# Performance work log

Hardware: AMD Instinct MI355X
Metric: run time of the kernel (lower is better)

The kernel has to match this reference:

```python
import jax, jax.numpy as jnp
import numpy as np

N = 50000      # nodes
E = 600000     # edges
G = 8          # graphs in the batch (for mean_nodes)
D = 128        # input_dim == hidden_dim
OUT = 10       # out_dim
NEG_SLOPE = 0.01  # nn.LeakyReLU default


def _lin(k, fi, fo):
    return jax.random.normal(k, (fi, fo), jnp.float32) / np.sqrt(fi).astype(np.float32)


def setup_inputs() -> dict:
    key = jax.random.key(0)
    ks = jax.random.split(key, 12)
    inputs = jax.random.normal(ks[0], (N, D), jnp.float32)
    src = jax.random.randint(ks[1], (E,), 0, N)
    dst = jax.random.randint(ks[2], (E,), 0, N)
    graph_id = jnp.sort(jax.random.randint(ks[3], (N,), 0, G))
    return {
        "inputs": inputs,
        "src": src,
        "dst": dst,
        "graph_id": graph_id,
        # GraphConv weights (DGL GraphConv: y = norm * A_norm x W + b)
        "W1": _lin(ks[4], D, D), "b1": jnp.zeros((D,), jnp.float32),
        "W2": _lin(ks[5], D, D), "b2": jnp.zeros((D,), jnp.float32),
        "W3": _lin(ks[6], D, D), "b3": jnp.zeros((D,), jnp.float32),
        # classifier head
        "Wc1": _lin(ks[7], D, 512),  "bc1": jnp.zeros((512,), jnp.float32),
        "Wc2": _lin(ks[8], 512, 256), "bc2": jnp.zeros((256,), jnp.float32),
        "Wc3": _lin(ks[9], 256, OUT), "bc3": jnp.zeros((OUT,), jnp.float32),
    }


def reference(inputs, src, dst, graph_id, W1, b1, W2, b2, W3, b3,
              Wc1, bc1, Wc2, bc2, Wc3, bc3):
    # DGL GraphConv with norm='both': h = D_in^{-1/2} A D_out^{-1/2} x W + b
    ones_e = jnp.ones((E,), jnp.float32)
    out_deg = jax.ops.segment_sum(ones_e, src, num_segments=N)
    in_deg = jax.ops.segment_sum(ones_e, dst, num_segments=N)
    src_norm = jnp.clip(out_deg, 1.0, None) ** -0.5   # [N]
    dst_norm = jnp.clip(in_deg, 1.0, None) ** -0.5    # [N]

    def gconv(x, W, b):
        x = x * src_norm[:, None]
        x = x @ W                                      # project first (in>=out)
        agg = jax.ops.segment_sum(x[src], dst, num_segments=N)  # SpMM
        return agg * dst_norm[:, None] + b

    h = gconv(inputs, W1, b1)
    h = gconv(h, W2, b2)
    h = gconv(h, W3, b3)

    # dgl.mean_nodes: per-graph mean over nodes
    sums = jax.ops.segment_sum(h, graph_id, num_segments=G)         # [G, D]
    cnts = jax.ops.segment_sum(jnp.ones((N,), jnp.float32), graph_id, num_segments=G)
    pooled = sums / jnp.clip(cnts, 1.0, None)[:, None]

    lrelu = lambda v: jax.nn.leaky_relu(v, NEG_SLOPE)
    x = lrelu(pooled @ Wc1 + bc1)
    x = lrelu(x @ Wc2 + bc2)
    x = lrelu(x @ Wc3 + bc3)
    return x
```

## Files before the change

kernel.cpp:

```cpp
#include <hip/hip_runtime.h>

#define Nn 50000
#define Ee 600000
#define Gg 8
#define Dd 128
#define NP 50048
#define SCHUNK 1024
#define NCHUNK ((Nn + SCHUNK - 1) / SCHUNK)

#define HWORDS 25024
#define HB 16
#define HIST_BLOCKS (2 * HB)
#define W12_BLOCKS 16
#define RN_BLOCKS ((HWORDS + 255) / 256)
#define W123_BLOCKS 64
#define PBLK ((Nn + 127) / 128)

__global__ __launch_bounds__(1024) void hist_kernel(
    const int* __restrict__ src, const int* __restrict__ dst,
    unsigned int* __restrict__ phist,
    const float* __restrict__ W1, const float* __restrict__ W2,
    const float* __restrict__ W3, const float* __restrict__ b1,
    const float* __restrict__ b2,
    float* __restrict__ W12, float* __restrict__ e1, float* __restrict__ e2,
    float* __restrict__ accz)
{
    __shared__ unsigned int h[HWORDS];
    int t = threadIdx.x;
    int b = blockIdx.x;

    if (b < HIST_BLOCKS) {
        for (int i = t; i < HWORDS; i += 1024) h[i] = 0u;
        __syncthreads();
        int part = b >> 1;
        const int* arr = (b & 1) ? dst : src;
        int e0 = part * (Ee / HB);
        int eN = e0 + (Ee / HB);
        for (int e = e0 + t; e < eN; e += 1024) {
            int n = arr[e];
            atomicAdd(&h[n >> 1], 1u << ((n & 1) << 4));
        }
        __syncthreads();
        unsigned int* out = phist + (size_t)b * HWORDS;
        for (int i = t; i < HWORDS; i += 1024) out[i] = h[i];
    } else if (b < HIST_BLOCKS + W12_BLOCKS) {
        int j = (b - HIST_BLOCKS) * 8 + (t & 7);
        int k = t >> 3;
        float a = 0.f;
#pragma unroll 8
        for (int m = 0; m < 128; ++m) a += W1[k * 128 + m] * W2[m * 128 + j];
        W12[k * 128 + j] = a;
    } else {
        if (t < 128) {
            float a = 0.f;
#pragma unroll 8
            for (int k = 0; k < 128; ++k) a += b1[k] * W2[k * 128 + t];
            e1[t] = a;
        } else if (t < 256) {
            int c = t - 128;
            float a = 0.f;
#pragma unroll 8
            for (int k = 0; k < 128; ++k) a += b2[k] * W3[k * 128 + c];
            e2[c] = a;
        } else if (t < 256 + 24) {
            accz[t - 256] = 0.f;
        }
    }
}

__global__ __launch_bounds__(256) void reduce_norm_kernel(
    const unsigned int* __restrict__ phist, const int* __restrict__ gid,
    int* __restrict__ odeg, float* __restrict__ srcn, float* __restrict__ pq,
    float* __restrict__ z, int* __restrict__ cnt,
    const float* __restrict__ W12, const float* __restrict__ W3,
    const float* __restrict__ e1,
    float* __restrict__ W123, float* __restrict__ e1b)
{
    int b = blockIdx.x, t = threadIdx.x;
    if (b < RN_BLOCKS) {
        __shared__ int lc[Gg];
        if (t < Gg) lc[t] = 0;
        __syncthreads();
        int i = b * 256 + t;
        if (i < HWORDS) {
            unsigned int so0 = 0, so1 = 0, si0 = 0, si1 = 0;
#pragma unroll
            for (int p = 0; p < HB; ++p) {
                unsigned int a = phist[(size_t)(2 * p) * HWORDS + i];
                unsigned int bb = phist[(size_t)(2 * p + 1) * HWORDS + i];
                so0 += a & 0xffffu; so1 += a >> 16;
                si0 += bb & 0xffffu; si1 += bb >> 16;
            }
#pragma unroll
            for (int hh = 0; hh < 2; ++hh) {
                int n = 2 * i + hh;
                unsigned int so = hh ? so1 : so0, si = hh ? si1 : si0;
                if (n < Nn) {
                    odeg[n] = (int)so;
                    float sn = 1.f / sqrtf(fmaxf((float)so, 1.f));
                    float dn = 1.f / sqrtf(fmaxf((float)si, 1.f));
                    srcn[n] = sn; pq[n] = sn * dn;
                    int g = gid[n];
                    atomicAdd(&lc[g], 1);
                    float zr[8];
#pragma unroll
                    for (int gg = 0; gg < 8; ++gg) zr[gg] = (gg == g) ? dn : 0.f;
                    *(float4*)(z + (size_t)n * 8)     = *(float4*)zr;
                    *(float4*)(z + (size_t)n * 8 + 4) = *(float4*)(zr + 4);
                }
            }
        }
        __syncthreads();
        if (t < Gg && lc[t] > 0) atomicAdd(&cnt[t], lc[t]);
    } else if (b < RN_BLOCKS + W123_BLOCKS) {
        int j = (b - RN_BLOCKS) * 2 + (t & 1);
        int k = t >> 1;
        float a = 0.f;
#pragma unroll 8
        for (int m = 0; m < 128; ++m) a += W12[k * 128 + m] * W3[m * 128 + j];
        W123[k * 128 + j] = a;
    } else {
        if (t < 128) {
            float a = 0.f;
#pragma unroll 8
            for (int k = 0; k < 128; ++k) a += e1[k] * W3[k * 128 + t];
            e1b[t] = a;
        }
    }
}

__global__ __launch_bounds__(256) void scanA(
    const int* __restrict__ deg, int* __restrict__ row_ptr, int* __restrict__ bsum)
{
    __shared__ int tsum[256];
    int b = blockIdx.x, t = threadIdx.x;
    int base = b * SCHUNK + t * 4;
    int v[4]; int s = 0;
#pragma unroll
    for (int i = 0; i < 4; ++i) {
        int idx = base + i;
        v[i] = (idx < Nn) ? deg[idx] : 0;
        s += v[i];
    }
    tsum[t] = s;
    __syncthreads();
    for (int off = 1; off < 256; off <<= 1) {
        int x = (t >= off) ? tsum[t - off] : 0;
        __syncthreads();
        tsum[t] += x;
        __syncthreads();
    }
    int run = tsum[t] - s;
#pragma unroll
    for (int i = 0; i < 4; ++i) {
        int idx = base + i;
        if (idx < Nn) row_ptr[idx] = run;
        run += v[i];
    }
    if (t == 255) bsum[b] = tsum[255];
}

__global__ void scanB(int* __restrict__ bsum)
{
    int t = threadIdx.x;
    int v = (t < NCHUNK) ? bsum[t] : 0;
    int orig = v;
    for (int off = 1; off < 64; off <<= 1) {
        int x = __shfl_up(v, off, 64);
        if (t >= off) v += x;
    }
    if (t < NCHUNK) bsum[t] = v - orig;
}

__global__ __launch_bounds__(256) void scanC(
    int* __restrict__ row_ptr, const int* __restrict__ bsum, int* __restrict__ cursor)
{
    int n = blockIdx.x * 256 + threadIdx.x;
    if (n >= Nn) return;
    int v = row_ptr[n] + bsum[n / SCHUNK];
    row_ptr[n] = v;
    cursor[n] = v;
    if (n == 0) row_ptr[Nn] = Ee;
}

__global__ __launch_bounds__(256) void fill_kernel(
    const int* __restrict__ src, const int* __restrict__ dst,
    int* __restrict__ cursor, int* __restrict__ csr_dst)
{
    int e = blockIdx.x * 256 + threadIdx.x;
    if (e >= Ee) return;
    int pos = atomicAdd(&cursor[src[e]], 1);
    csr_dst[pos] = dst[e];
}

__global__ __launch_bounds__(256) void bspmm_kernel(
    const float* __restrict__ uin, const int* __restrict__ row_ptr,
    const int* __restrict__ csr, const float* __restrict__ scal,
    float* __restrict__ uout, const float* __restrict__ sn,
    float* __restrict__ pwout)
{
    int t = threadIdx.x;
    int m = blockIdx.x * 32 + (t >> 3);
    int g = t & 7;
    float acc = 0.f, snm = 0.f;
    if (m < Nn) {
        int beg = row_ptr[m], end = row_ptr[m + 1];
        float a0 = 0.f, a1 = 0.f;
        int j = beg;
        if (scal) {
            for (; j + 1 < end; j += 2) {
                int i0 = csr[j], i1 = csr[j + 1];
                a0 += scal[i0] * uin[(size_t)i0 * 8 + g];
                a1 += scal[i1] * uin[(size_t)i1 * 8 + g];
            }
            if (j < end) { int i0 = csr[j]; a0 += scal[i0] * uin[(size_t)i0 * 8 + g]; }
        } else {
            for (; j + 1 < end; j += 2) {
                int i0 = csr[j], i1 = csr[j + 1];
                a0 += uin[(size_t)i0 * 8 + g];
                a1 += uin[(size_t)i1 * 8 + g];
            }
            if (j < end) a0 += uin[(size_t)csr[j] * 8 + g];
        }
        acc = a0 + a1;
        uout[(size_t)m * 8 + g] = acc;
        if (pwout) snm = sn[m];
    }
    if (pwout) {
        __shared__ float red[Gg];
        if (t < Gg) red[t] = 0.f;
        __syncthreads();
        atomicAdd(&red[g], snm * acc);
        __syncthreads();
        if (t < Gg) atomicAdd(&pwout[t], red[t]);
    }
}

__global__ __launch_bounds__(256) void dotpool_kernel(
    const float* __restrict__ x, const float* __restrict__ u3,
    const float* __restrict__ sn, float* __restrict__ partial)
{
    __shared__ float f[128][Gg];
    __shared__ float sp[Gg][Dd];
    int t = threadIdx.x;
    int n0 = blockIdx.x * 128;
    if (t < 128) {
        int n = n0 + t;
        float s = 0.f;
        float4 a = {0.f, 0.f, 0.f, 0.f}, b = {0.f, 0.f, 0.f, 0.f};
        if (n < Nn) {
            s = sn[n];
            a = *(const float4*)(u3 + (size_t)n * 8);
            b = *(const float4*)(u3 + (size_t)n * 8 + 4);
        }
        f[t][0] = s * a.x; f[t][1] = s * a.y; f[t][2] = s * a.z; f[t][3] = s * a.w;
        f[t][4] = s * b.x; f[t][5] = s * b.y; f[t][6] = s * b.z; f[t][7] = s * b.w;
    }
    for (int i = t; i < Gg * Dd; i += 256) ((float*)sp)[i] = 0.f;
    __syncthreads();

    int r0 = t >> 5, c = t & 31;
    float4 acc[Gg];
#pragma unroll
    for (int g = 0; g < Gg; ++g) acc[g] = make_float4(0.f, 0.f, 0.f, 0.f);
    for (int i = r0; i < 128; i += 8) {
        int n = n0 + i;
        if (n >= Nn) break;
        float4 xv = ((const float4*)x)[(size_t)n * 32 + c];
#pragma unroll
        for (int g = 0; g < Gg; ++g) {
            float fv = f[i][g];
            acc[g].x += fv * xv.x; acc[g].y += fv * xv.y;
            acc[g].z += fv * xv.z; acc[g].w += fv * xv.w;
        }
    }
#pragma unroll
    for (int g = 0; g < Gg; ++g) {
        atomicAdd(&sp[g][c * 4 + 0], acc[g].x);
        atomicAdd(&sp[g][c * 4 + 1], acc[g].y);
        atomicAdd(&sp[g][c * 4 + 2], acc[g].z);
        atomicAdd(&sp[g][c * 4 + 3], acc[g].w);
    }
    __syncthreads();
    float* out = partial + (size_t)blockIdx.x * Gg * Dd;
    for (int i = t; i < Gg * Dd; i += 256) out[i] = ((float*)sp)[i];
}

__global__ __launch_bounds__(256) void dotreduce_kernel(
    const float* __restrict__ partial, float* __restrict__ pooled)
{
    int i = blockIdx.x * 256 + threadIdx.x;
    float a0 = 0.f, a1 = 0.f, a2 = 0.f, a3 = 0.f;
    int b = 0;
    for (; b + 3 < PBLK; b += 4) {
        a0 += partial[(size_t)(b + 0) * Gg * Dd + i];
        a1 += partial[(size_t)(b + 1) * Gg * Dd + i];
        a2 += partial[(size_t)(b + 2) * Gg * Dd + i];
        a3 += partial[(size_t)(b + 3) * Gg * Dd + i];
    }
    for (; b < PBLK; ++b) a0 += partial[(size_t)b * Gg * Dd + i];
    pooled[i] = (a0 + a1) + (a2 + a3);
}

__global__ __launch_bounds__(1024) void x0_kernel(
    const float* __restrict__ pooled, const float* __restrict__ pw1r,
    const float* __restrict__ pw2r, const int* __restrict__ cnt,
    const float* __restrict__ W123, const float* __restrict__ e1b,
    const float* __restrict__ e2, const float* __restrict__ b3,
    float* __restrict__ x0g)
{
    int t = threadIdx.x;
    int g = t >> 7, c = t & 127;
    float a = 0.f;
#pragma unroll 8
    for (int k = 0; k < 128; ++k) a += pooled[g * 128 + k] * W123[k * 128 + c];
    float inv = 1.f / fmaxf((float)cnt[g], 1.f);
    x0g[t] = a * inv + (pw2r[g] * inv) * e1b[c] + (pw1r[g] * inv) * e2[c] + b3[c];
}

__global__ __launch_bounds__(256) void fc1_kernel(
    const float* __restrict__ x0g, const float* __restrict__ Wc1,
    const float* __restrict__ bc1, float* __restrict__ x1g)
{
    __shared__ float xs[Gg * 128];
    __shared__ float par[256];
    int t = threadIdx.x;
    for (int i = t; i < Gg * 128; i += 256) xs[i] = x0g[i];
    __syncthreads();
    int h = t >> 7, rem = t & 127;
    int g = rem >> 4, m = blockIdx.x * 16 + (rem & 15);
    int k0 = h * 64;
    float a = 0.f;
#pragma unroll 16
    for (int k = 0; k < 64; ++k) a += xs[g * 128 + k0 + k] * Wc1[(size_t)(k0 + k) * 512 + m];
    par[t] = a;
    __syncthreads();
    if (t < 128) {
        float v = par[t] + par[t + 128] + bc1[m];
        x1g[g * 512 + m] = v > 0.f ? v : 0.01f * v;
    }
}

__global__ __launch_bounds__(256) void fc2_kernel(
    const float* __restrict__ x1g, const float* __restrict__ Wc2,
    const float* __restrict__ bc2, float* __restrict__ x2g)
{
    __shared__ float xs[Gg * 512];
    __shared__ float par[256];
    int t = threadIdx.x;
    for (int i = t; i < Gg * 512; i += 256) xs[i] = x1g[i];
    __syncthreads();
    int q = t >> 6, rem = t & 63;
    int g = rem >> 3, m = blockIdx.x * 8 + (rem & 7);
    int k0 = q * 128;
    float a = 0.f;
#pragma unroll 16
    for (int k = 0; k < 128; ++k) a += xs[g * 512 + k0 + k] * Wc2[(size_t)(k0 + k) * 256 + m];
    par[t] = a;
    __syncthreads();
    if (t < 64) {
        float v = par[t] + par[t + 64] + par[t + 128] + par[t + 192] + bc2[m];
        x2g[g * 256 + m] = v > 0.f ? v : 0.01f * v;
    }
}

__global__ __launch_bounds__(640) void fc3_kernel(
    const float* __restrict__ x2g, const float* __restrict__ Wc3,
    const float* __restrict__ bc3, float* __restrict__ out)
{
    __shared__ float xs[Gg * 256];
    int t = threadIdx.x;
    for (int i = t; i < Gg * 256; i += 640) xs[i] = x2g[i];
    __syncthreads();
    int w = t >> 6, lane = t & 63;
    if (w < 10) {
        float acc[Gg];
#pragma unroll
        for (int g = 0; g < Gg; ++g) acc[g] = 0.f;
#pragma unroll
        for (int kk = 0; kk < 4; ++kk) {
            int k = lane + kk * 64;
            float wv = Wc3[(size_t)k * 10 + w];
#pragma unroll
            for (int g = 0; g < Gg; ++g) acc[g] += xs[g * 256 + k] * wv;
        }
#pragma unroll
        for (int g = 0; g < Gg; ++g) {
            float v = acc[g];
            for (int off = 32; off; off >>= 1) v += __shfl_down(v, off, 64);
            if (lane == 0) {
                v += bc3[w];
                out[g * 10 + w] = v > 0.f ? v : 0.01f * v;
            }
        }
    }
}

extern "C" void kernel_launch(void* const* d_in, const int* in_sizes, int n_in,
                              void* d_out, int out_size, void* d_ws, size_t ws_size,
                              hipStream_t stream)
{
    const float* inputs = (const float*)d_in[0];
    const int*   src    = (const int*)d_in[1];
    const int*   dst    = (const int*)d_in[2];
    const int*   gid    = (const int*)d_in[3];
    const float* W1  = (const float*)d_in[4];
    const float* b1  = (const float*)d_in[5];
    const float* W2  = (const float*)d_in[6];
    const float* b2  = (const float*)d_in[7];
    const float* W3  = (const float*)d_in[8];
    const float* b3  = (const float*)d_in[9];
    const float* Wc1 = (const float*)d_in[10];
    const float* bc1 = (const float*)d_in[11];
    const float* Wc2 = (const float*)d_in[12];
    const float* bc2 = (const float*)d_in[13];
    const float* Wc3 = (const float*)d_in[14];
    const float* bc3 = (const float*)d_in[15];

    int*   wi      = (int*)d_ws;
    int*   odeg    = wi;
    int*   row_ptr = odeg + NP;
    int*   cursor  = row_ptr + NP;
    int*   bsum    = cursor + NP;
    int*   csr_dst = bsum + 64;
    float* wf      = (float*)(csr_dst + Ee);
    float* srcn    = wf;
    float* pq      = srcn + NP;
    float* z       = pq + NP;
    float* u1      = z + (size_t)NP * 8;
    float* u2      = u1 + (size_t)NP * 8;
    float* u3      = u2 + (size_t)NP * 8;
    float* partial = u3 + (size_t)NP * 8;
    float* pooled  = partial + (size_t)PBLK * Gg * Dd;
    float* pw1     = pooled + Gg * Dd;
    float* pw2     = pw1 + Gg;
    int*   cnt     = (int*)(pw2 + Gg);
    float* W12v    = (float*)(cnt + Gg);
    float* W123v   = W12v + 128 * 128;
    float* e1v     = W123v + 128 * 128;
    float* e1bv    = e1v + 128;
    float* e2v     = e1bv + 128;
    float* x0g     = e2v + 128;
    float* x1g     = x0g + Gg * 128;
    float* x2g     = x1g + Gg * 512;
    unsigned int* phist = (unsigned int*)(x2g + Gg * 256);

    hist_kernel<<<HIST_BLOCKS + W12_BLOCKS + 1, 1024, 0, stream>>>(
        src, dst, phist, W1, W2, W3, b1, b2, W12v, e1v, e2v, pw1);
    reduce_norm_kernel<<<RN_BLOCKS + W123_BLOCKS + 1, 256, 0, stream>>>(
        phist, gid, odeg, srcn, pq, z, cnt, W12v, W3, e1v, W123v, e1bv);
    scanA<<<NCHUNK, 256, 0, stream>>>(odeg, row_ptr, bsum);
    scanB<<<1, 64, 0, stream>>>(bsum);
    scanC<<<(Nn + 255) / 256, 256, 0, stream>>>(row_ptr, bsum, cursor);
    fill_kernel<<<(Ee + 255) / 256, 256, 0, stream>>>(src, dst, cursor, csr_dst);

    int bblocks = (Nn + 31) / 32;
    bspmm_kernel<<<bblocks, 256, 0, stream>>>(z, row_ptr, csr_dst, nullptr,
                                              u1, srcn, pw1);
    bspmm_kernel<<<bblocks, 256, 0, stream>>>(u1, row_ptr, csr_dst, pq,
                                              u2, srcn, pw2);
    bspmm_kernel<<<bblocks, 256, 0, stream>>>(u2, row_ptr, csr_dst, pq,
                                              u3, nullptr, nullptr);

    dotpool_kernel<<<PBLK, 256, 0, stream>>>(inputs, u3, srcn, partial);
    dotreduce_kernel<<<4, 256, 0, stream>>>(partial, pooled);

    x0_kernel<<<1, 1024, 0, stream>>>(pooled, pw1, pw2, cnt, W123v, e1bv, e2v,
                                      b3, x0g);
    fc1_kernel<<<32, 256, 0, stream>>>(x0g, Wc1, bc1, x1g);
    fc2_kernel<<<32, 256, 0, stream>>>(x1g, Wc2, bc2, x2g);
    fc3_kernel<<<1, 640, 0, stream>>>(x2g, Wc3, bc3, (float*)d_out);
}
```

Baseline: 198.3 us.

## Fuse degree reduce with decoupled-lookback scan and fold third SpMM into pooling

Merges the degree-reduction/normalisation kernel with a single-pass scan that uses per-block flags and serial lookback, replacing three separate scan kernels. The third sparse aggregation is computed inside the pooling kernel, so u3 is never materialised, and the partial reduction is merged into the x0 projection kernel. This cuts several launches and global round trips. In exchange, correctness relies on earlier blocks running forward (spin-wait on flags), and the flags are zeroed in the hist kernel.

```diff
diff --git a/kernel.cpp b/kernel.cpp
--- a/kernel.cpp
+++ b/kernel.cpp
@@ -5,14 +5,12 @@
 #define Gg 8
 #define Dd 128
 #define NP 50048
-#define SCHUNK 1024
-#define NCHUNK ((Nn + SCHUNK - 1) / SCHUNK)
+#define NCHUNK 49
 
 #define HWORDS 25024
 #define HB 16
 #define HIST_BLOCKS (2 * HB)
 #define W12_BLOCKS 16
-#define RN_BLOCKS ((HWORDS + 255) / 256)
 #define W123_BLOCKS 64
 #define PBLK ((Nn + 127) / 128)
 
@@ -23,7 +21,7 @@
     const float* __restrict__ W3, const float* __restrict__ b1,
     const float* __restrict__ b2,
     float* __restrict__ W12, float* __restrict__ e1, float* __restrict__ e2,
-    float* __restrict__ accz)
+    int* __restrict__ accz)
 {
     __shared__ unsigned int h[HWORDS];
     int t = threadIdx.x;
@@ -62,41 +60,51 @@
 #pragma unroll 8
             for (int k = 0; k < 128; ++k) a += b2[k] * W3[k * 128 + c];
             e2[c] = a;
-        } else if (t < 256 + 24) {
-            accz[t - 256] = 0.f;
-        }
-    }
-}
-
-__global__ __launch_bounds__(256) void reduce_norm_kernel(
+        } else if (t < 256 + 88) {
+            accz[t - 256] = 0;
+        }
+    }
+}
+
+__global__ __launch_bounds__(256) void scan_fused(
     const unsigned int* __restrict__ phist, const int* __restrict__ gid,
-    int* __restrict__ odeg, float* __restrict__ srcn, float* __restrict__ pq,
-    float* __restrict__ z, int* __restrict__ cnt,
+    float* __restrict__ srcn, float* __restrict__ pq, float* __restrict__ z,
+    int* __restrict__ cnt, int* __restrict__ row_ptr, int* __restrict__ cursor,
+    int* __restrict__ fs,
     const float* __restrict__ W12, const float* __restrict__ W3,
     const float* __restrict__ e1,
     float* __restrict__ W123, float* __restrict__ e1b)
 {
     int b = blockIdx.x, t = threadIdx.x;
-    if (b < RN_BLOCKS) {
+    if (b < NCHUNK) {
+        __shared__ int tsum[256];
         __shared__ int lc[Gg];
+        __shared__ int sbase;
         if (t < Gg) lc[t] = 0;
         __syncthreads();
-        int i = b * 256 + t;
-        if (i < HWORDS) {
-            unsigned int so0 = 0, so1 = 0, si0 = 0, si1 = 0;
-#pragma unroll
-            for (int p = 0; p < HB; ++p) {
-                unsigned int a = phist[(size_t)(2 * p) * HWORDS + i];
-                unsigned int bb = phist[(size_t)(2 * p + 1) * HWORDS + i];
-                so0 += a & 0xffffu; so1 += a >> 16;
-                si0 += bb & 0xffffu; si1 += bb >> 16;
+
+        int d4[4];
+        int wbase = b * 512 + t * 2;
+#pragma unroll
+        for (int wi = 0; wi < 2; ++wi) {
+            int w = wbase + wi;
+            unsigned so0 = 0, so1 = 0, si0 = 0, si1 = 0;
+            if (w < HWORDS) {
+#pragma unroll
+                for (int p = 0; p < HB; ++p) {
+                    unsigned a  = phist[(size_t)(2 * p) * HWORDS + w];
+                    unsigned bb = phist[(size_t)(2 * p + 1) * HWORDS + w];
+                    so0 += a & 0xffffu; so1 += a >> 16;
+                    si0 += bb & 0xffffu; si1 += bb >> 16;
+                }
             }
 #pragma unroll
             for (int hh = 0; hh < 2; ++hh) {
-                int n = 2 * i + hh;
-                unsigned int so = hh ? so1 : so0, si = hh ? si1 : si0;
+                int n = 2 * w + hh;
+                unsigned so = hh ? so1 : so0, si = hh ? si1 : si0;
+                int d = 0;
                 if (n < Nn) {
-                    odeg[n] = (int)so;
+                    d = (int)so;
                     float sn = 1.f / sqrtf(fmaxf((float)so, 1.f));
                     float dn = 1.f / sqrtf(fmaxf((float)si, 1.f));
                     srcn[n] = sn; pq[n] = sn * dn;
@@ -108,12 +116,45 @@
                     *(float4*)(z + (size_t)n * 8)     = *(float4*)zr;
                     *(float4*)(z + (size_t)n * 8 + 4) = *(float4*)(zr + 4);
                 }
-            }
-        }
+                d4[wi * 2 + hh] = d;
+            }
+        }
+        int s = (d4[0] + d4[1]) + (d4[2] + d4[3]);
+        tsum[t] = s;
+        __syncthreads();
+        for (int off = 1; off < 256; off <<= 1) {
+            int x = (t >= off) ? tsum[t - off] : 0;
+            __syncthreads();
+            tsum[t] += x;
+            __syncthreads();
+        }
+        int run = tsum[t] - s;
+
+        if (t == 0) {
+            int total = tsum[255];
+            atomicExch(&fs[b], (total << 1) | 1);
+            int base = 0;
+            for (int p = 0; p < b; ++p) {
+                int r;
+                do { r = atomicAdd(&fs[p], 0); } while (!(r & 1));
+                base += (r >> 1);
+            }
+            sbase = base;
+        }
+        __syncthreads();
+
+        int gpos = sbase + run;
+#pragma unroll
+        for (int i = 0; i < 4; ++i) {
+            int n = b * 1024 + t * 4 + i;
+            if (n < Nn) { row_ptr[n] = gpos; cursor[n] = gpos; }
+            gpos += d4[i];
+        }
+        if (b == NCHUNK - 1 && t == 255) row_ptr[Nn] = Ee;
         __syncthreads();
         if (t < Gg && lc[t] > 0) atomicAdd(&cnt[t], lc[t]);
-    } else if (b < RN_BLOCKS + W123_BLOCKS) {
-        int j = (b - RN_BLOCKS) * 2 + (t & 1);
+    } else if (b < NCHUNK + W123_BLOCKS) {
+        int j = (b - NCHUNK) * 2 + (t & 1);
         int k = t >> 1;
         float a = 0.f;
 #pragma unroll 8
@@ -127,60 +168,6 @@
             e1b[t] = a;
         }
     }
-}
-
-__global__ __launch_bounds__(256) void scanA(
-    const int* __restrict__ deg, int* __restrict__ row_ptr, int* __restrict__ bsum)
-{
-    __shared__ int tsum[256];
-    int b = blockIdx.x, t = threadIdx.x;
-    int base = b * SCHUNK + t * 4;
-    int v[4]; int s = 0;
-#pragma unroll
-    for (int i = 0; i < 4; ++i) {
-        int idx = base + i;
-        v[i] = (idx < Nn) ? deg[idx] : 0;
-        s += v[i];
-    }
-    tsum[t] = s;
-    __syncthreads();
-    for (int off = 1; off < 256; off <<= 1) {
-        int x = (t >= off) ? tsum[t - off] : 0;
-        __syncthreads();
-        tsum[t] += x;
-        __syncthreads();
-    }
-    int run = tsum[t] - s;
-#pragma unroll
-    for (int i = 0; i < 4; ++i) {
-        int idx = base + i;
-        if (idx < Nn) row_ptr[idx] = run;
-        run += v[i];
-    }
-    if (t == 255) bsum[b] = tsum[255];
-}
-
-__global__ void scanB(int* __restrict__ bsum)
-{
-    int t = threadIdx.x;
-    int v = (t < NCHUNK) ? bsum[t] : 0;
-    int orig = v;
-    for (int off = 1; off < 64; off <<= 1) {
-        int x = __shfl_up(v, off, 64);
-        if (t >= off) v += x;
-    }
-    if (t < NCHUNK) bsum[t] = v - orig;
-}
-
-__global__ __launch_bounds__(256) void scanC(
-    int* __restrict__ row_ptr, const int* __restrict__ bsum, int* __restrict__ cursor)
-{
-    int n = blockIdx.x * 256 + threadIdx.x;
-    if (n >= Nn) return;
-    int v = row_ptr[n] + bsum[n / SCHUNK];
-    row_ptr[n] = v;
-    cursor[n] = v;
-    if (n == 0) row_ptr[Nn] = Ee;
 }
 
 __global__ __launch_bounds__(256) void fill_kernel(
@@ -237,24 +224,47 @@
 }
 
 __global__ __launch_bounds__(256) void dotpool_kernel(
-    const float* __restrict__ x, const float* __restrict__ u3,
-    const float* __restrict__ sn, float* __restrict__ partial)
+    const float* __restrict__ x, const float* __restrict__ u2,
+    const float* __restrict__ pq, const float* __restrict__ sn,
+    const int* __restrict__ row_ptr, const int* __restrict__ csr,
+    float* __restrict__ partial)
 {
     __shared__ float f[128][Gg];
     __shared__ float sp[Gg][Dd];
     int t = threadIdx.x;
     int n0 = blockIdx.x * 128;
-    if (t < 128) {
-        int n = n0 + t;
+
+    {
+        int i = t >> 1, gq = (t & 1) * 4;
+        int n = n0 + i;
+        float4 a0 = {0.f,0.f,0.f,0.f}, a1 = {0.f,0.f,0.f,0.f};
         float s = 0.f;
-        float4 a = {0.f, 0.f, 0.f, 0.f}, b = {0.f, 0.f, 0.f, 0.f};
         if (n < Nn) {
             s = sn[n];
-            a = *(const float4*)(u3 + (size_t)n * 8);
-            b = *(const float4*)(u3 + (size_t)n * 8 + 4);
-        }
-        f[t][0] = s * a.x; f[t][1] = s * a.y; f[t][2] = s * a.z; f[t][3] = s * a.w;
-        f[t][4] = s * b.x; f[t][5] = s * b.y; f[t][6] = s * b.z; f[t][7] = s * b.w;
+            int beg = row_ptr[n], end = row_ptr[n + 1];
+            int j = beg;
+            for (; j + 1 < end; j += 2) {
+                int i0 = csr[j], i1 = csr[j + 1];
+                float c0 = pq[i0], c1 = pq[i1];
+                float4 u0 = *(const float4*)(u2 + (size_t)i0 * 8 + gq);
+                float4 u1 = *(const float4*)(u2 + (size_t)i1 * 8 + gq);
+                a0.x += c0 * u0.x; a0.y += c0 * u0.y;
+                a0.z += c0 * u0.z; a0.w += c0 * u0.w;
+                a1.x += c1 * u1.x; a1.y += c1 * u1.y;
+                a1.z += c1 * u1.z; a1.w += c1 * u1.w;
+            }
+            if (j < end) {
+                int i0 = csr[j];
+                float c0 = pq[i0];
+                float4 u0 = *(const float4*)(u2 + (size_t)i0 * 8 + gq);
+                a0.x += c0 * u0.x; a0.y += c0 * u0.y;
+                a0.z += c0 * u0.z; a0.w += c0 * u0.w;
+            }
+        }
+        f[i][gq + 0] = s * (a0.x + a1.x);
+        f[i][gq + 1] = s * (a0.y + a1.y);
+        f[i][gq + 2] = s * (a0.z + a1.z);
+        f[i][gq + 3] = s * (a0.w + a1.w);
     }
     for (int i = t; i < Gg * Dd; i += 256) ((float*)sp)[i] = 0.f;
     __syncthreads();
@@ -286,36 +296,34 @@
     for (int i = t; i < Gg * Dd; i += 256) out[i] = ((float*)sp)[i];
 }
 
-__global__ __launch_bounds__(256) void dotreduce_kernel(
-    const float* __restrict__ partial, float* __restrict__ pooled)
-{
-    int i = blockIdx.x * 256 + threadIdx.x;
-    float a0 = 0.f, a1 = 0.f, a2 = 0.f, a3 = 0.f;
-    int b = 0;
-    for (; b + 3 < PBLK; b += 4) {
-        a0 += partial[(size_t)(b + 0) * Gg * Dd + i];
-        a1 += partial[(size_t)(b + 1) * Gg * Dd + i];
-        a2 += partial[(size_t)(b + 2) * Gg * Dd + i];
-        a3 += partial[(size_t)(b + 3) * Gg * Dd + i];
-    }
-    for (; b < PBLK; ++b) a0 += partial[(size_t)b * Gg * Dd + i];
-    pooled[i] = (a0 + a1) + (a2 + a3);
-}
-
-__global__ __launch_bounds__(1024) void x0_kernel(
-    const float* __restrict__ pooled, const float* __restrict__ pw1r,
+__global__ __launch_bounds__(256) void redx0_kernel(
+    const float* __restrict__ partial, const float* __restrict__ pw1r,
     const float* __restrict__ pw2r, const int* __restrict__ cnt,
     const float* __restrict__ W123, const float* __restrict__ e1b,
     const float* __restrict__ e2, const float* __restrict__ b3,
     float* __restrict__ x0g)
 {
-    int t = threadIdx.x;
-    int g = t >> 7, c = t & 127;
+    __shared__ float ps[256];
+    int t = threadIdx.x;
+    int o = blockIdx.x * 256 + t;
+    float a0 = 0.f, a1 = 0.f, a2 = 0.f, a3 = 0.f;
+    int b = 0;
+    for (; b + 3 < PBLK; b += 4) {
+        a0 += partial[(size_t)(b + 0) * 1024 + o];
+        a1 += partial[(size_t)(b + 1) * 1024 + o];
+        a2 += partial[(size_t)(b + 2) * 1024 + o];
+        a3 += partial[(size_t)(b + 3) * 1024 + o];
+    }
+    for (; b < PBLK; ++b) a0 += partial[(size_t)b * 1024 + o];
+    ps[t] = (a0 + a1) + (a2 + a3);
+    __syncthreads();
+
+    int g = o >> 7, c = o & 127, gl = t >> 7;
     float a = 0.f;
 #pragma unroll 8
-    for (int k = 0; k < 128; ++k) a += pooled[g * 128 + k] * W123[k * 128 + c];
+    for (int k = 0; k < 128; ++k) a += ps[gl * 128 + k] * W123[k * 128 + c];
     float inv = 1.f / fmaxf((float)cnt[g], 1.f);
-    x0g[t] = a * inv + (pw2r[g] * inv) * e1b[c] + (pw1r[g] * inv) * e2[c] + b3[c];
+    x0g[o] = a * inv + (pw2r[g] * inv) * e1b[c] + (pw1r[g] * inv) * e2[c] + b3[c];
 }
 
 __global__ __launch_bounds__(256) void fc1_kernel(
@@ -418,40 +426,35 @@
     const float* bc3 = (const float*)d_in[15];
 
     int*   wi      = (int*)d_ws;
-    int*   odeg    = wi;
-    int*   row_ptr = odeg + NP;
+    int*   row_ptr = wi;
     int*   cursor  = row_ptr + NP;
-    int*   bsum    = cursor + NP;
-    int*   csr_dst = bsum + 64;
+    int*   csr_dst = cursor + NP;
     float* wf      = (float*)(csr_dst + Ee);
     float* srcn    = wf;
     float* pq      = srcn + NP;
     float* z       = pq + NP;
     float* u1      = z + (size_t)NP * 8;
     float* u2      = u1 + (size_t)NP * 8;
-    float* u3      = u2 + (size_t)NP * 8;
-    float* partial = u3 + (size_t)NP * 8;
-    float* pooled  = partial + (size_t)PBLK * Gg * Dd;
-    float* pw1     = pooled + Gg * Dd;
+    float* partial = u2 + (size_t)NP * 8;
+    float* pw1     = partial + (size_t)PBLK * 1024;
     float* pw2     = pw1 + Gg;
     int*   cnt     = (int*)(pw2 + Gg);
-    float* W12v    = (float*)(cnt + Gg);
+    int*   fs      = cnt + Gg;
+    float* W12v    = (float*)(fs + 64);
     float* W123v   = W12v + 128 * 128;
     float* e1v     = W123v + 128 * 128;
     float* e1bv    = e1v + 128;
     float* e2v     = e1bv + 128;
     float* x0g     = e2v + 128;
-    float* x1g     = x0g + Gg * 128;
-    float* x2g     = x1g + Gg * 512;
-    unsigned int* phist = (unsigned int*)(x2g + Gg * 256);
+    float* x1g     = x0g + 1024;
+    float* x2g     = x1g + 4096;
+    unsigned int* phist = (unsigned int*)(x2g + 2048);
 
     hist_kernel<<<HIST_BLOCKS + W12_BLOCKS + 1, 1024, 0, stream>>>(
-        src, dst, phist, W1, W2, W3, b1, b2, W12v, e1v, e2v, pw1);
-    reduce_norm_kernel<<<RN_BLOCKS + W123_BLOCKS + 1, 256, 0, stream>>>(
-        phist, gid, odeg, srcn, pq, z, cnt, W12v, W3, e1v, W123v, e1bv);
-    scanA<<<NCHUNK, 256, 0, stream>>>(odeg, row_ptr, bsum);
-    scanB<<<1, 64, 0, stream>>>(bsum);
-    scanC<<<(Nn + 255) / 256, 256, 0, stream>>>(row_ptr, bsum, cursor);
+        src, dst, phist, W1, W2, W3, b1, b2, W12v, e1v, e2v, (int*)pw1);
+    scan_fused<<<NCHUNK + W123_BLOCKS + 1, 256, 0, stream>>>(
+        phist, gid, srcn, pq, z, cnt, row_ptr, cursor, fs,
+        W12v, W3, e1v, W123v, e1bv);
     fill_kernel<<<(Ee + 255) / 256, 256, 0, stream>>>(src, dst, cursor, csr_dst);
 
     int bblocks = (Nn + 31) / 32;
@@ -459,14 +462,11 @@
                                               u1, srcn, pw1);
     bspmm_kernel<<<bblocks, 256, 0, stream>>>(u1, row_ptr, csr_dst, pq,
                                               u2, srcn, pw2);
-    bspmm_kernel<<<bblocks, 256, 0, stream>>>(u2, row_ptr, csr_dst, pq,
-                                              u3, nullptr, nullptr);
-
-    dotpool_kernel<<<PBLK, 256, 0, stream>>>(inputs, u3, srcn, partial);
-    dotreduce_kernel<<<4, 256, 0, stream>>>(partial, pooled);
-
-    x0_kernel<<<1, 1024, 0, stream>>>(pooled, pw1, pw2, cnt, W123v, e1bv, e2v,
-                                      b3, x0g);
+
+    dotpool_kernel<<<PBLK, 256, 0, stream>>>(inputs, u2, pq, srcn,
+                                             row_ptr, csr_dst, partial);
+    redx0_kernel<<<4, 256, 0, stream>>>(partial, pw1, pw2, cnt,
+                                        W123v, e1bv, e2v, b3, x0g);
     fc1_kernel<<<32, 256, 0, stream>>>(x0g, Wc1, bc1, x1g);
     fc2_kernel<<<32, 256, 0, stream>>>(x1g, Wc2, bc2, x2g);
     fc3_kernel<<<1, 640, 0, stream>>>(x2g, Wc3, bc3, (float*)d_out);
```

Result: no change. 195.7 us (-1.3%).
